# Kernel optimization log

Measured on AMD Instinct MI355X. Metric: run time of the kernel, lower is better.

## Reference

```python
import jax, jax.numpy as jnp
import numpy as np

N_NODES = 100000
N_EDGES = 1600000
D = 64            # embedding_dim
D2 = D * D        # GRUCell hidden/input size


def gru_cell(x, h, w_ih, w_hh, b_ih, b_hh):
    # PyTorch GRUCell math. x, h: [D2]; w_ih, w_hh: [3*D2, D2]; b_*: [3*D2]
    gi = w_ih @ x + b_ih
    gh = w_hh @ h + b_hh
    i_r, i_z, i_n = jnp.split(gi, 3)
    h_r, h_z, h_n = jnp.split(gh, 3)
    r = jax.nn.sigmoid(i_r + h_r)
    z = jax.nn.sigmoid(i_z + h_z)
    n = jnp.tanh(i_n + r * h_n)
    return (1.0 - z) * n + z * h


def gcn_layer(x, w, src, dst, edge_norm):
    # dense transform then degree-normalized gather-scatter aggregation
    h = x @ w                                   # [N, D]
    m = h[src] * edge_norm[:, None]             # [E, D] messages
    return jax.ops.segment_sum(m, dst, num_segments=N_NODES)


def setup_inputs() -> dict:
    key = jax.random.key(0)
    ks = jax.random.split(key, 12)
    s = 0.02  # keep GRU gates in a sane range
    return {
        "node_embeddings": jax.random.normal(ks[0], (N_NODES, D), jnp.float32),
        "gc1_weights": jax.random.normal(ks[1], (D, D), jnp.float32) * s,
        "gc2_weights": jax.random.normal(ks[2], (D, D), jnp.float32) * s,
        "gc1_hist": jax.random.normal(ks[3], (D, D), jnp.float32) * s,
        "gc2_hist": jax.random.normal(ks[4], (D, D), jnp.float32) * s,
        "w_ih": jax.random.normal(ks[5], (3 * D2, D2), jnp.float32) * s,
        "w_hh": jax.random.normal(ks[6], (3 * D2, D2), jnp.float32) * s,
        "b_ih": jax.random.normal(ks[7], (3 * D2,), jnp.float32) * s,
        "b_hh": jax.random.normal(ks[8], (3 * D2,), jnp.float32) * s,
        "src": jax.random.randint(ks[9], (N_EDGES,), 0, N_NODES, jnp.int32),
        "dst": jax.random.randint(ks[10], (N_EDGES,), 0, N_NODES, jnp.int32),
    }


def reference(node_embeddings, gc1_weights, gc2_weights, gc1_hist, gc2_hist,
              w_ih, w_hh, b_ih, b_hh, src, dst):
    # --- weight evolution (GRUCell over flattened GCN weights) ---
    w1 = gru_cell(gc1_hist.reshape(-1), gc1_weights.reshape(-1),
                  w_ih, w_hh, b_ih, b_hh).reshape(D, D)
    w2 = gru_cell(gc2_hist.reshape(-1), gc2_weights.reshape(-1),
                  w_ih, w_hh, b_ih, b_hh).reshape(D, D)

    # --- symmetric degree normalization (in-degree, clamped at 1) ---
    deg = jax.ops.segment_sum(jnp.ones_like(dst, jnp.float32), dst,
                              num_segments=N_NODES)
    norm = jnp.clip(deg, 1.0, None) ** -0.5     # [N]
    edge_norm = norm[src] * norm[dst]           # [E]

    # --- two GCN layers ---
    x = jax.nn.relu(gcn_layer(node_embeddings, w1, src, dst, edge_norm))
    x = gcn_layer(x, w2, src, dst, edge_norm)
    return x
```

## Files before the change

kernel.cpp:

```cpp
#include <hip/hip_runtime.h>

typedef unsigned int uint_t;
typedef float v4f __attribute__((ext_vector_type(4)));

#define N_NODES 100000
#define N_EDGES 1600000
#define D 64
#define D2 4096
#define D3 12288

#define NPAD 100352u

#define BSHIFT 9
#define BNODES 512
#define NBUCK 196
#define CHUNK 8192
#define CAP   16384
#define GRUBLK 3072

#define OFF_GI1   0u
#define OFF_GI2   (OFF_GI1 + D3)
#define OFF_GH1   (OFF_GI2 + D3)
#define OFF_GH2   (OFF_GH1 + D3)
#define OFF_W1    (OFF_GH2 + D3)
#define OFF_W2    (OFF_W1 + D2)
#define OFF_DEG   (OFF_W2 + D2)
#define OFF_BCUR  (OFF_DEG + NPAD)
#define OFF_NORM  (OFF_BCUR + 256u)
#define OFF_ROWS  (OFF_NORM + NPAD)
#define OFF_CSR   (OFF_ROWS + NPAD)
#define OFF_H     (OFF_CSR + 1600000u)
#define OFF_AGG1  (OFF_H + 3200000u)
#define OFF_PAIRS (OFF_AGG1 + 6400000u)

__device__ __forceinline__ float dot4v(v4f a, float4 b, float acc) {
    acc = fmaf(a[0], b.x, acc);
    acc = fmaf(a[1], b.y, acc);
    acc = fmaf(a[2], b.z, acc);
    acc = fmaf(a[3], b.w, acc);
    return acc;
}

__device__ __forceinline__ uint_t bfr(float f) {
    uint_t u = __float_as_uint(f);
    u += 0x7FFFu + ((u >> 16) & 1u);
    return u >> 16;
}

struct PartLds {
    int hist[256];
    int lbase[256];
    int gbase[256];
    int lcur[256];
    int2 stage[CHUNK];
};
struct GruLds {
    float4 sA[1024];
    float4 sB[1024];
};

__global__ __launch_bounds__(512) void mega1(
    const float* __restrict__ w_ih, const float* __restrict__ w_hh,
    const float* __restrict__ x1, const float* __restrict__ x2,
    const float* __restrict__ h1, const float* __restrict__ h2,
    float* __restrict__ gi1, float* __restrict__ gi2,
    float* __restrict__ gh1, float* __restrict__ gh2,
    const int* __restrict__ src, const int* __restrict__ dst,
    int* __restrict__ deg, int* __restrict__ bcur, int2* __restrict__ pairs)
{
    __shared__ __align__(16) char ldsraw[sizeof(PartLds)];
    const int tid = threadIdx.x;

    if (blockIdx.x < NBUCK) {
        PartLds& P = *reinterpret_cast<PartLds*>(ldsraw);
        const int e0  = blockIdx.x * CHUNK;
        const int cnt = min(CHUNK, N_EDGES - e0);

        if (tid < 256) { P.hist[tid] = 0; P.lcur[tid] = 0; }
        __syncthreads();
        for (int i = tid; i < cnt; i += 512) {
            const int d = dst[e0 + i];
            atomicAdd(&deg[d], 1);
            atomicAdd(&P.hist[d >> BSHIFT], 1);
        }
        __syncthreads();
        if (tid < 256) P.lbase[tid] = P.hist[tid];
        __syncthreads();
        for (int off = 1; off < 256; off <<= 1) {
            int a = 0, b = 0;
            if (tid < 256) { a = P.lbase[tid]; b = (tid >= off) ? P.lbase[tid - off] : 0; }
            __syncthreads();
            if (tid < 256) P.lbase[tid] = a + b;
            __syncthreads();
        }
        if (tid < 256) {
            const int c = P.hist[tid];
            P.lbase[tid] -= c;
            P.gbase[tid] = c ? atomicAdd(&bcur[tid], c) : 0;
        }
        __syncthreads();
        for (int i = tid; i < cnt; i += 512) {
            const int s = src[e0 + i], d = dst[e0 + i];
            const int b = d >> BSHIFT;
            const int p = P.lbase[b] + atomicAdd(&P.lcur[b], 1);
            P.stage[p] = make_int2(s, d);
        }
        __syncthreads();
        for (int i = tid; i < cnt; i += 512) {
            const int2 v = P.stage[i];
            const int b = v.y >> BSHIFT;
            const int gp = P.gbase[b] + (i - P.lbase[b]);
            if (gp < CAP) pairs[(size_t)b * CAP + gp] = v;
        }
    } else {
        GruLds& G = *reinterpret_cast<GruLds*>(ldsraw);
        const int gb   = blockIdx.x - NBUCK;
        const int half = (gb >= GRUBLK / 2);
        const int blk  = gb - (half ? GRUBLK / 2 : 0);

        {
            const float4* va = (const float4*)(half ? h1 : x1);
            const float4* vb = (const float4*)(half ? h2 : x2);
#pragma unroll
            for (int i = 0; i < 2; ++i) {
                const int k = tid + i * 512;
                G.sA[k] = va[k];
                G.sB[k] = vb[k];
            }
        }
        __syncthreads();

        const int wave = tid >> 6, lane = tid & 63;
        const int row  = blk * 8 + wave;
        const v4f* wr = (const v4f*)((half ? w_hh : w_ih) + (size_t)row * D2);

        float p0 = 0.f, p1 = 0.f;
#pragma unroll
        for (int g = 0; g < 4; ++g) {
            v4f a[4];
#pragma unroll
            for (int k = 0; k < 4; ++k)
                a[k] = __builtin_nontemporal_load(&wr[lane + (g * 4 + k) * 64]);
#pragma unroll
            for (int k = 0; k < 4; ++k) {
                const int idx = lane + (g * 4 + k) * 64;
                p0 = dot4v(a[k], G.sA[idx], p0);
                p1 = dot4v(a[k], G.sB[idx], p1);
            }
        }
#pragma unroll
        for (int m = 32; m > 0; m >>= 1) {
            p0 += __shfl_down(p0, m, 64);
            p1 += __shfl_down(p1, m, 64);
        }
        if (lane == 0) {
            float* oA = half ? gh1 : gi1;
            float* oB = half ? gh2 : gi2;
            oA[row] = p0;
            oB[row] = p1;
        }
    }
}

__global__ __launch_bounds__(256) void gates_norm_kernel(
    const float* __restrict__ gi1, const float* __restrict__ gh1,
    const float* __restrict__ gi2, const float* __restrict__ gh2,
    const float* __restrict__ b_ih, const float* __restrict__ b_hh,
    const float* __restrict__ hw1, const float* __restrict__ hw2,
    float* __restrict__ w1, float* __restrict__ w2,
    const int* __restrict__ deg, float* __restrict__ norm)
{
    const int blk = blockIdx.x;
    const int tid = threadIdx.x;
    if (blk < 32) {
        const int layer = blk >> 4;
        const int j = (blk & 15) * 256 + tid;
        const float* gi = layer ? gi2 : gi1;
        const float* gh = layer ? gh2 : gh1;
        const float* hw = layer ? hw2 : hw1;
        float* wo = layer ? w2 : w1;

        float ir = gi[j]          + b_ih[j];
        float hr = gh[j]          + b_hh[j];
        float iz = gi[j + D2]     + b_ih[j + D2];
        float hz = gh[j + D2]     + b_hh[j + D2];
        float in_ = gi[j + 2*D2]  + b_ih[j + 2*D2];
        float hn = gh[j + 2*D2]   + b_hh[j + 2*D2];

        float r = 1.f / (1.f + expf(-(ir + hr)));
        float z = 1.f / (1.f + expf(-(iz + hz)));
        float n = tanhf(in_ + r * hn);
        wo[j] = (1.f - z) * n + z * hw[j];
    } else {
        const int n = (blk - 32) * 256 + tid;
        if (n < N_NODES) norm[n] = 1.0f / sqrtf(fmaxf((float)deg[n], 1.0f));
    }
}

__global__ __launch_bounds__(256) void bucket_csr_kernel(
    const int2* __restrict__ pairs, const int* __restrict__ deg,
    const int* __restrict__ bcnt,
    int* __restrict__ rowstart, int* __restrict__ csr_src)
{
    __shared__ int lofs[BNODES];
    __shared__ int lcur[BNODES];
    __shared__ int pscan[256];
    __shared__ int bscan[256];
    __shared__ int stage[CAP];
    const int tid = threadIdx.x;
    const int b   = blockIdx.x;
    const int nodeBase = b << BSHIFT;

    const int cb = (tid < NBUCK) ? bcnt[tid] : 0;
    bscan[tid] = cb;
    __syncthreads();
    for (int off = 1; off < 256; off <<= 1) {
        int a = bscan[tid];
        int x = (tid >= off) ? bscan[tid - off] : 0;
        __syncthreads();
        bscan[tid] = a + x;
        __syncthreads();
    }
    const int cnt  = bcnt[b];
    const int base = bscan[b] - cnt;

    const int n0 = nodeBase + 2 * tid;
    const int d0 = (n0     < N_NODES) ? deg[n0]     : 0;
    const int d1 = (n0 + 1 < N_NODES) ? deg[n0 + 1] : 0;
    pscan[tid] = d0 + d1;
    __syncthreads();
    for (int off = 1; off < 256; off <<= 1) {
        int a = pscan[tid];
        int x = (tid >= off) ? pscan[tid - off] : 0;
        __syncthreads();
        pscan[tid] = a + x;
        __syncthreads();
    }
    const int ex = pscan[tid] - (d0 + d1);
    lofs[2 * tid]     = ex;
    lofs[2 * tid + 1] = ex + d0;
    lcur[2 * tid]     = 0;
    lcur[2 * tid + 1] = 0;

    if (n0     < N_NODES) rowstart[n0]     = base + ex;
    if (n0 + 1 < N_NODES) rowstart[n0 + 1] = base + ex + d0;
    __syncthreads();

    const int2* bp = pairs + (size_t)b * CAP;
    for (int i = tid; i < cnt; i += 256) {
        const int2 v = bp[i];
        const int ln = v.y - nodeBase;
        const int p  = lofs[ln] + atomicAdd(&lcur[ln], 1);
        stage[p] = v.x;
    }
    __syncthreads();
    for (int i = tid; i < cnt; i += 256)
        csr_src[base + i] = stage[i];
}

template <bool RELU>
__global__ __launch_bounds__(256) void transform_kernel(
    const float* __restrict__ xin, const float* __restrict__ w,
    const float* __restrict__ norm, unsigned short* __restrict__ outbf)
{
    __shared__ float sw[D * D];
    const int tid = threadIdx.x;
#pragma unroll
    for (int i = 0; i < 16; ++i) sw[tid + i * 256] = w[tid + i * 256];
    __syncthreads();

    const int node = blockIdx.x * 256 + tid;
    if (node >= N_NODES) return;

    float x[D];
    const float4* p = (const float4*)(xin + (size_t)node * D);
#pragma unroll
    for (int i = 0; i < 16; ++i) {
        float4 u = p[i];
        x[i * 4 + 0] = u.x; x[i * 4 + 1] = u.y;
        x[i * 4 + 2] = u.z; x[i * 4 + 3] = u.w;
    }
    if (RELU) {
#pragma unroll
        for (int k = 0; k < D; ++k) x[k] = fmaxf(x[k], 0.f);
    }

    float acc[D];
#pragma unroll
    for (int j = 0; j < D; ++j) acc[j] = 0.f;
#pragma unroll
    for (int k = 0; k < D; ++k) {
        float a = x[k];
#pragma unroll
        for (int j = 0; j < D; ++j) acc[j] = fmaf(a, sw[k * D + j], acc[j]);
    }

    const float nn = norm[node];
    uint_t pk[32];
#pragma unroll
    for (int j = 0; j < 32; ++j)
        pk[j] = bfr(acc[2 * j] * nn) | (bfr(acc[2 * j + 1] * nn) << 16);

    uint4* po = (uint4*)(outbf + (size_t)node * D);
#pragma unroll
    for (int i = 0; i < 8; ++i)
        po[i] = make_uint4(pk[4 * i], pk[4 * i + 1], pk[4 * i + 2], pk[4 * i + 3]);
}

__global__ __launch_bounds__(256) void aggregate_gather(
    const unsigned short* __restrict__ hbf, const int* __restrict__ csr_src,
    const int* __restrict__ rowstart, const int* __restrict__ degv,
    const float* __restrict__ norm, float* __restrict__ out)
{
    const int tid  = threadIdx.x;
    const int node = blockIdx.x * 16 + (tid >> 4);
    if (node >= N_NODES) return;
    const int lg = tid & 15;
    const uint2* hp = (const uint2*)hbf;

    const int beg = rowstart[node];
    const int dg  = degv[node];

    float4 acc = make_float4(0.f, 0.f, 0.f, 0.f);
    int k = 0;
    for (; k + 8 <= dg; k += 8) {
        int s[8];
#pragma unroll
        for (int u = 0; u < 8; ++u) s[u] = csr_src[beg + k + u];
        uint2 r[8];
#pragma unroll
        for (int u = 0; u < 8; ++u) r[u] = hp[(size_t)s[u] * 16 + lg];
#pragma unroll
        for (int u = 0; u < 8; ++u) {
            acc.x += __uint_as_float(r[u].x << 16);
            acc.y += __uint_as_float(r[u].x & 0xFFFF0000u);
            acc.z += __uint_as_float(r[u].y << 16);
            acc.w += __uint_as_float(r[u].y & 0xFFFF0000u);
        }
    }
    for (; k < dg; ++k) {
        const int s = csr_src[beg + k];
        const uint2 r = hp[(size_t)s * 16 + lg];
        acc.x += __uint_as_float(r.x << 16);
        acc.y += __uint_as_float(r.x & 0xFFFF0000u);
        acc.z += __uint_as_float(r.y << 16);
        acc.w += __uint_as_float(r.y & 0xFFFF0000u);
    }

    const float nn = norm[node];
    float4 o = make_float4(acc.x * nn, acc.y * nn, acc.z * nn, acc.w * nn);
    *(float4*)(out + (size_t)node * D + (size_t)lg * 4) = o;
}

extern "C" void kernel_launch(void* const* d_in, const int* in_sizes, int n_in,
                              void* d_out, int out_size, void* d_ws, size_t ws_size,
                              hipStream_t stream)
{
    const float* emb  = (const float*)d_in[0];
    const float* gc1w = (const float*)d_in[1];
    const float* gc2w = (const float*)d_in[2];
    const float* gc1h = (const float*)d_in[3];
    const float* gc2h = (const float*)d_in[4];
    const float* w_ih = (const float*)d_in[5];
    const float* w_hh = (const float*)d_in[6];
    const float* b_ih = (const float*)d_in[7];
    const float* b_hh = (const float*)d_in[8];
    const int* src = (const int*)d_in[9];
    const int* dst = (const int*)d_in[10];

    float* ws = (float*)d_ws;
    float* gi1 = ws + OFF_GI1;
    float* gi2 = ws + OFF_GI2;
    float* gh1 = ws + OFF_GH1;
    float* gh2 = ws + OFF_GH2;
    float* w1  = ws + OFF_W1;
    float* w2  = ws + OFF_W2;
    int*   deg = (int*)(ws + OFF_DEG);
    int*   bcur = (int*)(ws + OFF_BCUR);
    float* nrm = ws + OFF_NORM;
    int*   rows = (int*)(ws + OFF_ROWS);
    int*   csr  = (int*)(ws + OFF_CSR);
    unsigned short* hbf = (unsigned short*)(ws + OFF_H);
    float* agg1 = ws + OFF_AGG1;
    int2*  pairs = (int2*)(ws + OFF_PAIRS);
    float* out  = (float*)d_out;

    hipMemsetAsync(deg, 0, (NPAD + 256) * sizeof(int), stream);

    mega1<<<NBUCK + GRUBLK, 512, 0, stream>>>(
        w_ih, w_hh, gc1h, gc2h, gc1w, gc2w, gi1, gi2, gh1, gh2,
        src, dst, deg, bcur, pairs);

    gates_norm_kernel<<<32 + (N_NODES + 255) / 256, 256, 0, stream>>>(
        gi1, gh1, gi2, gh2, b_ih, b_hh, gc1w, gc2w, w1, w2, deg, nrm);

    bucket_csr_kernel<<<NBUCK, 256, 0, stream>>>(pairs, deg, bcur, rows, csr);

    transform_kernel<false><<<(N_NODES + 255) / 256, 256, 0, stream>>>(emb, w1, nrm, hbf);
    aggregate_gather<<<(N_NODES + 15) / 16, 256, 0, stream>>>(hbf, csr, rows, deg, nrm, agg1);

    transform_kernel<true><<<(N_NODES + 255) / 256, 256, 0, stream>>>(agg1, w2, nrm, hbf);
    aggregate_gather<<<(N_NODES + 15) / 16, 256, 0, stream>>>(hbf, csr, rows, deg, nrm, out);
}
```

Measured before the change: 608.8 us.

## Fuse GRU gates into transform, compute norm inline, store layer-1 output as bf16

Removes the separate gates/norm kernel. Each transform block now recomputes the GRU gate math for the full 64x64 weight while filling shared memory, and both the transform and aggregate kernels compute the degree normalization inline with rsqrt. The intermediate layer-1 aggregate is written as bf16 with ReLU already applied, which halves its write and read traffic. The cost is redundant gate computation in every one of roughly 391 blocks, about 12 extra global loads per weight element, plus an extra bf16 rounding of the intermediate activations.

```diff
diff --git a/kernel.cpp b/kernel.cpp
--- a/kernel.cpp
+++ b/kernel.cpp
@@ -22,16 +22,13 @@
 #define OFF_GI2   (OFF_GI1 + D3)
 #define OFF_GH1   (OFF_GI2 + D3)
 #define OFF_GH2   (OFF_GH1 + D3)
-#define OFF_W1    (OFF_GH2 + D3)
-#define OFF_W2    (OFF_W1 + D2)
-#define OFF_DEG   (OFF_W2 + D2)
+#define OFF_DEG   (OFF_GH2 + D3)
 #define OFF_BCUR  (OFF_DEG + NPAD)
-#define OFF_NORM  (OFF_BCUR + 256u)
-#define OFF_ROWS  (OFF_NORM + NPAD)
+#define OFF_ROWS  (OFF_BCUR + 256u)
 #define OFF_CSR   (OFF_ROWS + NPAD)
 #define OFF_H     (OFF_CSR + 1600000u)
 #define OFF_AGG1  (OFF_H + 3200000u)
-#define OFF_PAIRS (OFF_AGG1 + 6400000u)
+#define OFF_PAIRS (OFF_AGG1 + 3200000u)
 
 __device__ __forceinline__ float dot4v(v4f a, float4 b, float acc) {
     acc = fmaf(a[0], b.x, acc);
@@ -159,41 +156,6 @@
             oA[row] = p0;
             oB[row] = p1;
         }
-    }
-}
-
-__global__ __launch_bounds__(256) void gates_norm_kernel(
-    const float* __restrict__ gi1, const float* __restrict__ gh1,
-    const float* __restrict__ gi2, const float* __restrict__ gh2,
-    const float* __restrict__ b_ih, const float* __restrict__ b_hh,
-    const float* __restrict__ hw1, const float* __restrict__ hw2,
-    float* __restrict__ w1, float* __restrict__ w2,
-    const int* __restrict__ deg, float* __restrict__ norm)
-{
-    const int blk = blockIdx.x;
-    const int tid = threadIdx.x;
-    if (blk < 32) {
-        const int layer = blk >> 4;
-        const int j = (blk & 15) * 256 + tid;
-        const float* gi = layer ? gi2 : gi1;
-        const float* gh = layer ? gh2 : gh1;
-        const float* hw = layer ? hw2 : hw1;
-        float* wo = layer ? w2 : w1;
-
-        float ir = gi[j]          + b_ih[j];
-        float hr = gh[j]          + b_hh[j];
-        float iz = gi[j + D2]     + b_ih[j + D2];
-        float hz = gh[j + D2]     + b_hh[j + D2];
-        float in_ = gi[j + 2*D2]  + b_ih[j + 2*D2];
-        float hn = gh[j + 2*D2]   + b_hh[j + 2*D2];
-
-        float r = 1.f / (1.f + expf(-(ir + hr)));
-        float z = 1.f / (1.f + expf(-(iz + hz)));
-        float n = tanhf(in_ + r * hn);
-        wo[j] = (1.f - z) * n + z * hw[j];
-    } else {
-        const int n = (blk - 32) * 256 + tid;
-        if (n < N_NODES) norm[n] = 1.0f / sqrtf(fmaxf((float)deg[n], 1.0f));
     }
 }
 
@@ -258,31 +220,58 @@
         csr_src[base + i] = stage[i];
 }
 
-template <bool RELU>
+template <bool BF16IN>
 __global__ __launch_bounds__(256) void transform_kernel(
-    const float* __restrict__ xin, const float* __restrict__ w,
-    const float* __restrict__ norm, unsigned short* __restrict__ outbf)
+    const void* __restrict__ xin,
+    const float* __restrict__ gi, const float* __restrict__ gh,
+    const float* __restrict__ b_ih, const float* __restrict__ b_hh,
+    const float* __restrict__ hw,
+    const int* __restrict__ deg, unsigned short* __restrict__ outbf)
 {
     __shared__ float sw[D * D];
     const int tid = threadIdx.x;
 #pragma unroll
-    for (int i = 0; i < 16; ++i) sw[tid + i * 256] = w[tid + i * 256];
+    for (int i = 0; i < 16; ++i) {
+        const int j = tid + i * 256;
+        float ir = gi[j]          + b_ih[j];
+        float hr = gh[j]          + b_hh[j];
+        float iz = gi[j + D2]     + b_ih[j + D2];
+        float hz = gh[j + D2]     + b_hh[j + D2];
+        float in_ = gi[j + 2*D2]  + b_ih[j + 2*D2];
+        float hn = gh[j + 2*D2]   + b_hh[j + 2*D2];
+        float r = 1.f / (1.f + expf(-(ir + hr)));
+        float z = 1.f / (1.f + expf(-(iz + hz)));
+        float n = tanhf(in_ + r * hn);
+        sw[j] = (1.f - z) * n + z * hw[j];
+    }
     __syncthreads();
 
     const int node = blockIdx.x * 256 + tid;
     if (node >= N_NODES) return;
 
     float x[D];
-    const float4* p = (const float4*)(xin + (size_t)node * D);
-#pragma unroll
-    for (int i = 0; i < 16; ++i) {
-        float4 u = p[i];
-        x[i * 4 + 0] = u.x; x[i * 4 + 1] = u.y;
-        x[i * 4 + 2] = u.z; x[i * 4 + 3] = u.w;
-    }
-    if (RELU) {
-#pragma unroll
-        for (int k = 0; k < D; ++k) x[k] = fmaxf(x[k], 0.f);
+    if (BF16IN) {
+        const uint4* p = (const uint4*)((const unsigned short*)xin + (size_t)node * D);
+#pragma unroll
+        for (int i = 0; i < 8; ++i) {
+            uint4 u = p[i];
+            x[i*8+0] = __uint_as_float(u.x << 16);
+            x[i*8+1] = __uint_as_float(u.x & 0xFFFF0000u);
+            x[i*8+2] = __uint_as_float(u.y << 16);
+            x[i*8+3] = __uint_as_float(u.y & 0xFFFF0000u);
+            x[i*8+4] = __uint_as_float(u.z << 16);
+            x[i*8+5] = __uint_as_float(u.z & 0xFFFF0000u);
+            x[i*8+6] = __uint_as_float(u.w << 16);
+            x[i*8+7] = __uint_as_float(u.w & 0xFFFF0000u);
+        }
+    } else {
+        const float4* p = (const float4*)((const float*)xin + (size_t)node * D);
+#pragma unroll
+        for (int i = 0; i < 16; ++i) {
+            float4 u = p[i];
+            x[i*4+0] = u.x; x[i*4+1] = u.y;
+            x[i*4+2] = u.z; x[i*4+3] = u.w;
+        }
     }
 
     float acc[D];
@@ -295,7 +284,7 @@
         for (int j = 0; j < D; ++j) acc[j] = fmaf(a, sw[k * D + j], acc[j]);
     }
 
-    const float nn = norm[node];
+    const float nn = rsqrtf(fmaxf((float)deg[node], 1.0f));
     uint_t pk[32];
 #pragma unroll
     for (int j = 0; j < 32; ++j)
@@ -307,10 +296,11 @@
         po[i] = make_uint4(pk[4 * i], pk[4 * i + 1], pk[4 * i + 2], pk[4 * i + 3]);
 }
 
+template <bool BF16RELU_OUT>
 __global__ __launch_bounds__(256) void aggregate_gather(
     const unsigned short* __restrict__ hbf, const int* __restrict__ csr_src,
     const int* __restrict__ rowstart, const int* __restrict__ degv,
-    const float* __restrict__ norm, float* __restrict__ out)
+    void* __restrict__ out)
 {
     const int tid  = threadIdx.x;
     const int node = blockIdx.x * 16 + (tid >> 4);
@@ -347,9 +337,20 @@
         acc.w += __uint_as_float(r.y & 0xFFFF0000u);
     }
 
-    const float nn = norm[node];
-    float4 o = make_float4(acc.x * nn, acc.y * nn, acc.z * nn, acc.w * nn);
-    *(float4*)(out + (size_t)node * D + (size_t)lg * 4) = o;
+    const float nn = rsqrtf(fmaxf((float)dg, 1.0f));
+    if (BF16RELU_OUT) {
+        const float ox = fmaxf(acc.x * nn, 0.f);
+        const float oy = fmaxf(acc.y * nn, 0.f);
+        const float oz = fmaxf(acc.z * nn, 0.f);
+        const float ow = fmaxf(acc.w * nn, 0.f);
+        uint2 pk;
+        pk.x = bfr(ox) | (bfr(oy) << 16);
+        pk.y = bfr(oz) | (bfr(ow) << 16);
+        ((uint2*)out)[(size_t)node * 16 + lg] = pk;
+    } else {
+        float4 o = make_float4(acc.x * nn, acc.y * nn, acc.z * nn, acc.w * nn);
+        *(float4*)((float*)out + (size_t)node * D + (size_t)lg * 4) = o;
+    }
 }
 
 extern "C" void kernel_launch(void* const* d_in, const int* in_sizes, int n_in,
@@ -373,15 +374,12 @@
     float* gi2 = ws + OFF_GI2;
     float* gh1 = ws + OFF_GH1;
     float* gh2 = ws + OFF_GH2;
-    float* w1  = ws + OFF_W1;
-    float* w2  = ws + OFF_W2;
     int*   deg = (int*)(ws + OFF_DEG);
     int*   bcur = (int*)(ws + OFF_BCUR);
-    float* nrm = ws + OFF_NORM;
     int*   rows = (int*)(ws + OFF_ROWS);
     int*   csr  = (int*)(ws + OFF_CSR);
-    unsigned short* hbf = (unsigned short*)(ws + OFF_H);
-    float* agg1 = ws + OFF_AGG1;
+    unsigned short* hbf  = (unsigned short*)(ws + OFF_H);
+    unsigned short* agg1 = (unsigned short*)(ws + OFF_AGG1);
     int2*  pairs = (int2*)(ws + OFF_PAIRS);
     float* out  = (float*)d_out;
 
@@ -391,14 +389,15 @@
         w_ih, w_hh, gc1h, gc2h, gc1w, gc2w, gi1, gi2, gh1, gh2,
         src, dst, deg, bcur, pairs);
 
-    gates_norm_kernel<<<32 + (N_NODES + 255) / 256, 256, 0, stream>>>(
-        gi1, gh1, gi2, gh2, b_ih, b_hh, gc1w, gc2w, w1, w2, deg, nrm);
-
     bucket_csr_kernel<<<NBUCK, 256, 0, stream>>>(pairs, deg, bcur, rows, csr);
 
-    transform_kernel<false><<<(N_NODES + 255) / 256, 256, 0, stream>>>(emb, w1, nrm, hbf);
-    aggregate_gather<<<(N_NODES + 15) / 16, 256, 0, stream>>>(hbf, csr, rows, deg, nrm, agg1);
-
-    transform_kernel<true><<<(N_NODES + 255) / 256, 256, 0, stream>>>(agg1, w2, nrm, hbf);
-    aggregate_gather<<<(N_NODES + 15) / 16, 256, 0, stream>>>(hbf, csr, rows, deg, nrm, out);
-}
+    transform_kernel<false><<<(N_NODES + 255) / 256, 256, 0, stream>>>(
+        emb, gi1, gh1, b_ih, b_hh, gc1w, deg, hbf);
+    aggregate_gather<true><<<(N_NODES + 15) / 16, 256, 0, stream>>>(
+        hbf, csr, rows, deg, agg1);
+
+    transform_kernel<true><<<(N_NODES + 255) / 256, 256, 0, stream>>>(
+        agg1, gi2, gh2, b_ih, b_hh, gc2w, deg, hbf);
+    aggregate_gather<false><<<(N_NODES + 15) / 16, 256, 0, stream>>>(
+        hbf, csr, rows, deg, out);
+}
```

Result: slower. 625.2 us (+2.7%).
